# Kernel optimization log

Measured on AMD Instinct MI355X. Metric: run time of the kernel, lower is better.

## Reference

```python
import jax, jax.numpy as jnp
import numpy as np

NUM_NODES = 100000
MAX_DEGREE = 128
NODE_DIM = 256
VERT_NUM = 16384
NUM_SAMPLES = 32


def setup_inputs() -> dict:
    key = jax.random.key(0)
    k1, k2, k3, k4, k5 = jax.random.split(key, 5)
    ids = jax.random.randint(k1, (VERT_NUM,), 0, NUM_NODES, dtype=jnp.int32)
    unif_rand = jax.random.randint(k2, (NUM_SAMPLES,), 0, MAX_DEGREE, dtype=jnp.int32)
    adj_info = jax.random.randint(k3, (NUM_NODES, MAX_DEGREE), 0, NUM_NODES, dtype=jnp.int32)
    features = jax.random.normal(k4, (NUM_NODES, NODE_DIM), dtype=jnp.float32)
    W = jax.random.normal(k5, (NODE_DIM, NODE_DIM), dtype=jnp.float32) / np.sqrt(NODE_DIM)
    b = jnp.zeros((NODE_DIM,), dtype=jnp.float32)
    return {"ids": ids, "unif_rand": unif_rand, "adj_info": adj_info,
            "features": features, "W": W, "b": b}


def reference(ids, unif_rand, adj_info, features, W, b):
    num_nodes = adj_info.shape[0]
    sentinel = num_nodes - 1  # padding / "no neighbor" id

    # gather neighbor lists for the batch, then subsample columns uniformly
    adj_lists = adj_info[ids]                 # [V, max_degree]
    adj_lists = adj_lists[:, unif_rand]       # [V, S]

    # gather features
    v_f = features[ids]                       # [V, D]
    n_f = features[adj_lists]                 # [V, S, D]

    # linear sampler branch: dense projection then batched dot with neighbors
    l = v_f @ W + b                           # [V, D]
    out = jax.nn.relu(jnp.einsum('vd,vsd->vs', l, n_f))  # [V, S]

    out_mean = jnp.mean(out, axis=1)          # [V]

    # drop neighbors that are the sentinel or whose score exceeds 0.5*mean
    condition = (adj_lists == sentinel) | (out > 0.5 * out_mean[:, None])
    adj_out = jnp.where(condition, jnp.int32(sentinel), adj_lists)     # [V, S]
    adj_lists_numnz = jnp.sum(jnp.where(condition, 0.0, 1.0), axis=1)  # [V]
    att_lists = jnp.ones(adj_out.shape, dtype=jnp.float32)

    return adj_out, att_lists, adj_lists_numnz, out_mean
```

## Files before the change

kernel.cpp:

```cpp
#include <hip/hip_runtime.h>

#define NUM_NODES 100000
#define MAX_DEGREE 128
#define NODE_DIM 256
#define VERT_NUM 16384
#define NUM_SAMPLES 32
#define SENTINEL (NUM_NODES - 1)

#define VPB 8
#define NBLK (VERT_NUM / VPB)

#define ADJ_OFF 0
#define ATT_OFF (VERT_NUM * NUM_SAMPLES)
#define NNZ_OFF (2 * VERT_NUM * NUM_SAMPLES)
#define MEAN_OFF (2 * VERT_NUM * NUM_SAMPLES + VERT_NUM)

__device__ __forceinline__ float bfbits2f(unsigned int bits16) {
    return __uint_as_float(bits16 << 16);
}

__device__ __forceinline__ int probe_isf32(const void* p) {
    const unsigned int* fu = (const unsigned int*)p;
    int cnt = 0;
    for (int i = 0; i < 64; ++i) {
        const unsigned int w = fu[i];
        const unsigned int e2 = (w >> 7) & 0xFFu;
        if (e2 >= 90u && e2 <= 140u && (w & 0xFFFFu) != 0u) ++cnt;
    }
    return (cnt >= 40) ? 0 : 1;
}

template <int ISF32>
__device__ __forceinline__ float ld1(const void* p, size_t idx) {
    if (ISF32) return ((const float*)p)[idx];
    return bfbits2f(((const unsigned short*)p)[idx]);
}

template <int ISF32>
__device__ __forceinline__ float4 load4(const void* p, size_t idx) {
    if (ISF32) {
        return *(const float4*)((const float*)p + idx);
    } else {
        const ushort4 u = *(const ushort4*)((const unsigned short*)p + idx);
        float4 v;
        v.x = bfbits2f(u.x); v.y = bfbits2f(u.y);
        v.z = bfbits2f(u.z); v.w = bfbits2f(u.w);
        return v;
    }
}

template <int ISF32>
__device__ __forceinline__ void body(
    const int* __restrict__ adj_info,
    const void* __restrict__ features,
    const void* __restrict__ W,
    const void* __restrict__ bias,
    float* __restrict__ out,
    float (*AL_s)[NODE_DIM + 4],
    const int* s_ids,
    const int* s_ur,
    int (*s_adj)[NUM_SAMPLES],
    float (*s_out)[NUM_SAMPLES],
    int tid, int v0)
{
    #pragma unroll
    for (int i = 0; i < 2; ++i) {
        const int idx = tid + i * 256;
        const int r = idx >> 6;
        const int cg = (idx & 63) * 4;
        const float4 v = load4<ISF32>(features, (size_t)s_ids[r] * NODE_DIM + cg);
        *(float4*)&AL_s[r][cg] = v;
    }
    {
        const int r = tid >> 5;
        const int s = tid & 31;
        s_adj[r][s] = adj_info[(size_t)s_ids[r] * MAX_DEGREE + s_ur[s]];
    }
    __syncthreads();

    double acc[VPB];
    {
        const int col = tid;
        #pragma unroll
        for (int g = 0; g < VPB; ++g) acc[g] = 0.0;
        float wn0 = ld1<ISF32>(W, (size_t)0 * NODE_DIM + col);
        float wn1 = ld1<ISF32>(W, (size_t)1 * NODE_DIM + col);
        float wn2 = ld1<ISF32>(W, (size_t)2 * NODE_DIM + col);
        float wn3 = ld1<ISF32>(W, (size_t)3 * NODE_DIM + col);
        #pragma unroll 2
        for (int k = 0; k < NODE_DIM; k += 4) {
            const double w0 = (double)wn0;
            const double w1 = (double)wn1;
            const double w2 = (double)wn2;
            const double w3 = (double)wn3;
            if (k + 4 < NODE_DIM) {
                wn0 = ld1<ISF32>(W, (size_t)(k + 4) * NODE_DIM + col);
                wn1 = ld1<ISF32>(W, (size_t)(k + 5) * NODE_DIM + col);
                wn2 = ld1<ISF32>(W, (size_t)(k + 6) * NODE_DIM + col);
                wn3 = ld1<ISF32>(W, (size_t)(k + 7) * NODE_DIM + col);
            }
            #pragma unroll
            for (int g = 0; g < VPB; ++g) {
                const float4 a = *(const float4*)&AL_s[g][k];
                acc[g] = fma((double)a.x, w0, acc[g]);
                acc[g] = fma((double)a.y, w1, acc[g]);
                acc[g] = fma((double)a.z, w2, acc[g]);
                acc[g] = fma((double)a.w, w3, acc[g]);
            }
        }
    }
    __syncthreads();
    {
        const int col = tid;
        const double bv = (double)ld1<ISF32>(bias, col);
        #pragma unroll
        for (int g = 0; g < VPB; ++g) AL_s[g][col] = (float)(acc[g] + bv);
    }
    __syncthreads();

    {
        const int q = tid >> 4;
        const int ln = tid & 15;
        const int g = q >> 1;
        const int so = (q & 1) * 16;
        const int ln4 = ln * 4;
        const float4 Lv0 = *(const float4*)&AL_s[g][  0 + ln4];
        const float4 Lv1 = *(const float4*)&AL_s[g][ 64 + ln4];
        const float4 Lv2 = *(const float4*)&AL_s[g][128 + ln4];
        const float4 Lv3 = *(const float4*)&AL_s[g][192 + ln4];
        const int* adjq = s_adj[g];

        float4 fA0, fA1, fA2, fA3, fB0, fB1, fB2, fB3;

#define EIN_LOAD(B0, B1, B2, B3, SIDX) do {                                 \
            const size_t b_ = (size_t)adjq[(SIDX)] * NODE_DIM + ln4;        \
            B0 = load4<ISF32>(features, b_ +   0);                          \
            B1 = load4<ISF32>(features, b_ +  64);                          \
            B2 = load4<ISF32>(features, b_ + 128);                          \
            B3 = load4<ISF32>(features, b_ + 192);                          \
        } while (0)

#define EIN_COMPUTE(B0, B1, B2, B3, SIDX) do {                              \
            double a_ = 0.0;                                                \
            a_ = fma((double)B0.x, (double)Lv0.x, a_);                      \
            a_ = fma((double)B0.y, (double)Lv0.y, a_);                      \
            a_ = fma((double)B0.z, (double)Lv0.z, a_);                      \
            a_ = fma((double)B0.w, (double)Lv0.w, a_);                      \
            a_ = fma((double)B1.x, (double)Lv1.x, a_);                      \
            a_ = fma((double)B1.y, (double)Lv1.y, a_);                      \
            a_ = fma((double)B1.z, (double)Lv1.z, a_);                      \
            a_ = fma((double)B1.w, (double)Lv1.w, a_);                      \
            a_ = fma((double)B2.x, (double)Lv2.x, a_);                      \
            a_ = fma((double)B2.y, (double)Lv2.y, a_);                      \
            a_ = fma((double)B2.z, (double)Lv2.z, a_);                      \
            a_ = fma((double)B2.w, (double)Lv2.w, a_);                      \
            a_ = fma((double)B3.x, (double)Lv3.x, a_);                      \
            a_ = fma((double)B3.y, (double)Lv3.y, a_);                      \
            a_ = fma((double)B3.z, (double)Lv3.z, a_);                      \
            a_ = fma((double)B3.w, (double)Lv3.w, a_);                      \
            a_ += __shfl_xor(a_, 8);                                        \
            a_ += __shfl_xor(a_, 4);                                        \
            a_ += __shfl_xor(a_, 2);                                        \
            a_ += __shfl_xor(a_, 1);                                        \
            if (ln == 0) s_out[g][(SIDX)] = (float)a_;                      \
        } while (0)

        EIN_LOAD(fA0, fA1, fA2, fA3, so + 0);
        #pragma unroll
        for (int si = 0; si < 16; si += 2) {
            EIN_LOAD(fB0, fB1, fB2, fB3, so + si + 1);
            EIN_COMPUTE(fA0, fA1, fA2, fA3, so + si);
            if (si + 2 < 16) EIN_LOAD(fA0, fA1, fA2, fA3, so + si + 2);
            EIN_COMPUTE(fB0, fB1, fB2, fB3, so + si + 1);
        }
#undef EIN_LOAD
#undef EIN_COMPUTE
    }
    __syncthreads();

    if (tid < VPB * 16) {
        const int q = tid >> 4;
        const int ln = tid & 15;
        const int v = v0 + q;
        const float o0 = fmaxf(s_out[q][ln], 0.0f);
        const float o1 = fmaxf(s_out[q][ln + 16], 0.0f);
        double ss = (double)o0 + (double)o1;
        ss += __shfl_xor(ss, 8);
        ss += __shfl_xor(ss, 4);
        ss += __shfl_xor(ss, 2);
        ss += __shfl_xor(ss, 1);
        const float mean = (float)(ss * (1.0 / 32.0));
        const float thr = 0.5f * mean;
        const int n0 = s_adj[q][ln];
        const int n1 = s_adj[q][ln + 16];
        const bool c0 = (n0 == SENTINEL) || (o0 > thr);
        const bool c1 = (n1 == SENTINEL) || (o1 > thr);
        const size_t ob = (size_t)v * NUM_SAMPLES;
        out[ADJ_OFF + ob + ln]      = c0 ? (float)SENTINEL : (float)n0;
        out[ADJ_OFF + ob + ln + 16] = c1 ? (float)SENTINEL : (float)n1;
        out[ATT_OFF + ob + ln]      = 1.0f;
        out[ATT_OFF + ob + ln + 16] = 1.0f;
        int nz = (c0 ? 0 : 1) + (c1 ? 0 : 1);
        nz += __shfl_xor(nz, 8);
        nz += __shfl_xor(nz, 4);
        nz += __shfl_xor(nz, 2);
        nz += __shfl_xor(nz, 1);
        if (ln == 0) {
            out[NNZ_OFF + v] = (float)nz;
            out[MEAN_OFF + v] = mean;
        }
    }
}

__global__ __launch_bounds__(256, 6)
void FastMLNeighborSampler___9337258901923_kernel(
    const int* ids,
    const int* unif_rand,
    const int* adj_info,
    const void* features_raw,
    const void* W_raw,
    const void* bias_raw,
    float* out) {
    __shared__ float AL_s[VPB][NODE_DIM + 4];
    __shared__ int s_ids[VPB];
    __shared__ int s_ur[NUM_SAMPLES];
    __shared__ int s_adj[VPB][NUM_SAMPLES];
    __shared__ float s_out[VPB][NUM_SAMPLES];
    __shared__ int s_isf32;

    const int tid = threadIdx.x;
    const int v0 = blockIdx.x * VPB;

    if (tid == 0) s_isf32 = probe_isf32(features_raw);
    if (tid < VPB) {
        s_ids[tid] = ids[v0 + tid];
    } else if (tid < VPB + NUM_SAMPLES) {
        s_ur[tid - VPB] = unif_rand[tid - VPB];
    }
    __syncthreads();

    if (s_isf32) {
        body<1>(adj_info, features_raw, W_raw, bias_raw, out,
                AL_s, s_ids, s_ur, s_adj, s_out, tid, v0);
    } else {
        body<0>(adj_info, features_raw, W_raw, bias_raw, out,
                AL_s, s_ids, s_ur, s_adj, s_out, tid, v0);
    }
}

extern "C" void kernel_launch(void* const* d_in, const int* in_sizes, int n_in,
                              void* d_out, int out_size, void* d_ws, size_t ws_size,
                              hipStream_t stream) {
    const int* ids = nullptr;
    const int* unif_rand = nullptr;
    const int* adj_info = nullptr;
    const void* features = nullptr;
    const void* W = nullptr;
    const void* bias = nullptr;
    for (int i = 0; i < n_in; ++i) {
        switch (in_sizes[i]) {
            case VERT_NUM:               ids       = (const int*)d_in[i]; break;
            case NUM_SAMPLES:            unif_rand = (const int*)d_in[i]; break;
            case NUM_NODES * MAX_DEGREE: adj_info  = (const int*)d_in[i]; break;
            case NUM_NODES * NODE_DIM:   features  = (const void*)d_in[i]; break;
            case NODE_DIM * NODE_DIM:    W         = (const void*)d_in[i]; break;
            case NODE_DIM:               bias      = (const void*)d_in[i]; break;
            default: break;
        }
    }
    if (!ids || !unif_rand || !adj_info || !features || !W || !bias) {
        ids       = (const int*)d_in[0];
        unif_rand = (const int*)d_in[1];
        adj_info  = (const int*)d_in[2];
        features  = (const void*)d_in[3];
        W         = (const void*)d_in[4];
        bias      = (const void*)d_in[5];
    }
    float* out = (float*)d_out;

    FastMLNeighborSampler___9337258901923_kernel<<<NBLK, 256, 0, stream>>>(
        ids, unif_rand, adj_info, features, W, bias, out);
}
```

Baseline: 270.8 us.

## Retile projection as 2 columns x 4 vertices per thread with double-precision LDS

Changes the projection GEMM mapping so each thread computes two output columns for four vertices instead of one column for eight vertices. This halves the per-block W loads, which are now float2 loads. Vertex features are pre-converted to double in shared memory through a union with the float output buffer, which removes the repeated float-to-double conversions in the inner loop. The cost is a larger shared-memory footprint (about 16KB), which may reduce occupancy.

```diff
diff --git a/kernel.cpp b/kernel.cpp
--- a/kernel.cpp
+++ b/kernel.cpp
@@ -34,6 +34,16 @@
 __device__ __forceinline__ float ld1(const void* p, size_t idx) {
     if (ISF32) return ((const float*)p)[idx];
     return bfbits2f(((const unsigned short*)p)[idx]);
+}
+
+template <int ISF32>
+__device__ __forceinline__ float2 load2(const void* p, size_t idx) {
+    if (ISF32) {
+        return *(const float2*)((const float*)p + idx);
+    } else {
+        const ushort2 u = *(const ushort2*)((const unsigned short*)p + idx);
+        return make_float2(bfbits2f(u.x), bfbits2f(u.y));
+    }
 }
 
 template <int ISF32>
@@ -49,6 +59,11 @@
     }
 }
 
+union ALUnion {
+    double ad[VPB][NODE_DIM + 2];
+    float  lf[VPB][NODE_DIM + 4];
+};
+
 template <int ISF32>
 __device__ __forceinline__ void body(
     const int* __restrict__ adj_info,
@@ -56,7 +71,7 @@
     const void* __restrict__ W,
     const void* __restrict__ bias,
     float* __restrict__ out,
-    float (*AL_s)[NODE_DIM + 4],
+    ALUnion* __restrict__ u,
     const int* s_ids,
     const int* s_ur,
     int (*s_adj)[NUM_SAMPLES],
@@ -64,12 +79,13 @@
     int tid, int v0)
 {
     #pragma unroll
-    for (int i = 0; i < 2; ++i) {
+    for (int i = 0; i < 4; ++i) {
         const int idx = tid + i * 256;
-        const int r = idx >> 6;
-        const int cg = (idx & 63) * 4;
-        const float4 v = load4<ISF32>(features, (size_t)s_ids[r] * NODE_DIM + cg);
-        *(float4*)&AL_s[r][cg] = v;
+        const int r = idx >> 7;
+        const int dc = (idx & 127) * 2;
+        const float2 v = load2<ISF32>(features, (size_t)s_ids[r] * NODE_DIM + dc);
+        u->ad[r][dc]     = (double)v.x;
+        u->ad[r][dc + 1] = (double)v.y;
     }
     {
         const int r = tid >> 5;
@@ -78,43 +94,54 @@
     }
     __syncthreads();
 
-    double acc[VPB];
     {
-        const int col = tid;
+        const int h  = tid >> 7;
+        const int c2 = (tid & 127) * 2;
+        const int g0 = h * 4;
+        double acc[4][2];
         #pragma unroll
-        for (int g = 0; g < VPB; ++g) acc[g] = 0.0;
-        float wn0 = ld1<ISF32>(W, (size_t)0 * NODE_DIM + col);
-        float wn1 = ld1<ISF32>(W, (size_t)1 * NODE_DIM + col);
-        float wn2 = ld1<ISF32>(W, (size_t)2 * NODE_DIM + col);
-        float wn3 = ld1<ISF32>(W, (size_t)3 * NODE_DIM + col);
+        for (int g = 0; g < 4; ++g) { acc[g][0] = 0.0; acc[g][1] = 0.0; }
+
+        float2 wn0 = load2<ISF32>(W, (size_t)0 * NODE_DIM + c2);
+        float2 wn1 = load2<ISF32>(W, (size_t)1 * NODE_DIM + c2);
+        float2 wn2 = load2<ISF32>(W, (size_t)2 * NODE_DIM + c2);
+        float2 wn3 = load2<ISF32>(W, (size_t)3 * NODE_DIM + c2);
         #pragma unroll 2
         for (int k = 0; k < NODE_DIM; k += 4) {
-            const double w0 = (double)wn0;
-            const double w1 = (double)wn1;
-            const double w2 = (double)wn2;
-            const double w3 = (double)wn3;
+            const double w00 = (double)wn0.x, w01 = (double)wn0.y;
+            const double w10 = (double)wn1.x, w11 = (double)wn1.y;
+            const double w20 = (double)wn2.x, w21 = (double)wn2.y;
+            const double w30 = (double)wn3.x, w31 = (double)wn3.y;
             if (k + 4 < NODE_DIM) {
-                wn0 = ld1<ISF32>(W, (size_t)(k + 4) * NODE_DIM + col);
-                wn1 = ld1<ISF32>(W, (size_t)(k + 5) * NODE_DIM + col);
-                wn2 = ld1<ISF32>(W, (size_t)(k + 6) * NODE_DIM + col);
-                wn3 = ld1<ISF32>(W, (size_t)(k + 7) * NODE_DIM + col);
+                wn0 = load2<ISF32>(W, (size_t)(k + 4) * NODE_DIM + c2);
+                wn1 = load2<ISF32>(W, (size_t)(k + 5) * NODE_DIM + c2);
+                wn2 = load2<ISF32>(W, (size_t)(k + 6) * NODE_DIM + c2);
+                wn3 = load2<ISF32>(W, (size_t)(k + 7) * NODE_DIM + c2);
             }
             #pragma unroll
-            for (int g = 0; g < VPB; ++g) {
-                const float4 a = *(const float4*)&AL_s[g][k];
-                acc[g] = fma((double)a.x, w0, acc[g]);
-                acc[g] = fma((double)a.y, w1, acc[g]);
-                acc[g] = fma((double)a.z, w2, acc[g]);
-                acc[g] = fma((double)a.w, w3, acc[g]);
+            for (int g = 0; g < 4; ++g) {
+                const double2 a01 = *(const double2*)&u->ad[g0 + g][k];
+                const double2 a23 = *(const double2*)&u->ad[g0 + g][k + 2];
+                acc[g][0] = fma(a01.x, w00, acc[g][0]);
+                acc[g][0] = fma(a01.y, w10, acc[g][0]);
+                acc[g][0] = fma(a23.x, w20, acc[g][0]);
+                acc[g][0] = fma(a23.y, w30, acc[g][0]);
+                acc[g][1] = fma(a01.x, w01, acc[g][1]);
+                acc[g][1] = fma(a01.y, w11, acc[g][1]);
+                acc[g][1] = fma(a23.x, w21, acc[g][1]);
+                acc[g][1] = fma(a23.y, w31, acc[g][1]);
             }
         }
-    }
-    __syncthreads();
-    {
-        const int col = tid;
-        const double bv = (double)ld1<ISF32>(bias, col);
-        #pragma unroll
-        for (int g = 0; g < VPB; ++g) AL_s[g][col] = (float)(acc[g] + bv);
+        __syncthreads();
+        {
+            const double b0 = (double)ld1<ISF32>(bias, c2);
+            const double b1 = (double)ld1<ISF32>(bias, (size_t)c2 + 1);
+            #pragma unroll
+            for (int g = 0; g < 4; ++g) {
+                u->lf[g0 + g][c2]     = (float)(acc[g][0] + b0);
+                u->lf[g0 + g][c2 + 1] = (float)(acc[g][1] + b1);
+            }
+        }
     }
     __syncthreads();
 
@@ -124,10 +151,10 @@
         const int g = q >> 1;
         const int so = (q & 1) * 16;
         const int ln4 = ln * 4;
-        const float4 Lv0 = *(const float4*)&AL_s[g][  0 + ln4];
-        const float4 Lv1 = *(const float4*)&AL_s[g][ 64 + ln4];
-        const float4 Lv2 = *(const float4*)&AL_s[g][128 + ln4];
-        const float4 Lv3 = *(const float4*)&AL_s[g][192 + ln4];
+        const float4 Lv0 = *(const float4*)&u->lf[g][  0 + ln4];
+        const float4 Lv1 = *(const float4*)&u->lf[g][ 64 + ln4];
+        const float4 Lv2 = *(const float4*)&u->lf[g][128 + ln4];
+        const float4 Lv3 = *(const float4*)&u->lf[g][192 + ln4];
         const int* adjq = s_adj[g];
 
         float4 fA0, fA1, fA2, fA3, fB0, fB1, fB2, fB3;
@@ -221,7 +248,7 @@
     const void* W_raw,
     const void* bias_raw,
     float* out) {
-    __shared__ float AL_s[VPB][NODE_DIM + 4];
+    __shared__ ALUnion uAL;
     __shared__ int s_ids[VPB];
     __shared__ int s_ur[NUM_SAMPLES];
     __shared__ int s_adj[VPB][NUM_SAMPLES];
@@ -241,10 +268,10 @@
 
     if (s_isf32) {
         body<1>(adj_info, features_raw, W_raw, bias_raw, out,
-                AL_s, s_ids, s_ur, s_adj, s_out, tid, v0);
+                &uAL, s_ids, s_ur, s_adj, s_out, tid, v0);
     } else {
         body<0>(adj_info, features_raw, W_raw, bias_raw, out,
-                AL_s, s_ids, s_ur, s_adj, s_out, tid, v0);
+                &uAL, s_ids, s_ur, s_adj, s_out, tid, v0);
     }
 }
 
```

Result: slower. 315.2 us (+16.4%).

## Warp-specialize block into matmul and gather-einsum pipeline stages with double buffering

Applied to the files above, without the earlier changes.

Each block now handles 16 vertices in two tiles of 8 and runs 512 threads. Warps 0-3 compute the dense projection for tile t while warps 4-7 do the neighbor-gather dot products and the thresholding for tile t-1, with double-buffered shared memory for the inputs and projections. The epilogue is folded into the einsum warps using a ballot/popcount instead of a separate pass. This aims to overlap the FP64 matmul with the memory-bound feature gathers. The cost is that each group idles during the pipeline fill and drain, the block uses more shared memory, and there are half as many blocks.

```diff
diff --git a/kernel.cpp b/kernel.cpp
--- a/kernel.cpp
+++ b/kernel.cpp
@@ -7,8 +7,11 @@
 #define NUM_SAMPLES 32
 #define SENTINEL (NUM_NODES - 1)
 
-#define VPB 8
-#define NBLK (VERT_NUM / VPB)
+#define TVPB 8
+#define TILES 2
+#define VPBLK (TVPB * TILES)
+#define NBLK (VERT_NUM / VPBLK)
+#define NTHR 512
 
 #define ADJ_OFF 0
 #define ATT_OFF (VERT_NUM * NUM_SAMPLES)
@@ -51,168 +54,191 @@
 
 template <int ISF32>
 __device__ __forceinline__ void body(
+    const int* __restrict__ ids,
     const int* __restrict__ adj_info,
     const void* __restrict__ features,
     const void* __restrict__ W,
     const void* __restrict__ bias,
     float* __restrict__ out,
-    float (*AL_s)[NODE_DIM + 4],
-    const int* s_ids,
+    float (*bufA)[TVPB][NODE_DIM + 4],
+    float (*bufL)[TVPB][NODE_DIM + 4],
+    int (*s_adj)[TVPB][NUM_SAMPLES],
     const int* s_ur,
-    int (*s_adj)[NUM_SAMPLES],
-    float (*s_out)[NUM_SAMPLES],
-    int tid, int v0)
+    int tid, int v_blk)
 {
-    #pragma unroll
-    for (int i = 0; i < 2; ++i) {
-        const int idx = tid + i * 256;
-        const int r = idx >> 6;
-        const int cg = (idx & 63) * 4;
-        const float4 v = load4<ISF32>(features, (size_t)s_ids[r] * NODE_DIM + cg);
-        *(float4*)&AL_s[r][cg] = v;
-    }
     {
-        const int r = tid >> 5;
-        const int s = tid & 31;
-        s_adj[r][s] = adj_info[(size_t)s_ids[r] * MAX_DEGREE + s_ur[s]];
-    }
+        const int r = tid >> 6;
+        const int cg = (tid & 63) * 4;
+        const float4 v = load4<ISF32>(features, (size_t)ids[v_blk + r] * NODE_DIM + cg);
+        *(float4*)&bufA[0][r][cg] = v;
+        if (tid < 256) {
+            const int rr = tid >> 5;
+            const int ss = tid & 31;
+            s_adj[0][rr][ss] = adj_info[(size_t)ids[v_blk + rr] * MAX_DEGREE + s_ur[ss]];
+        }
+    }
+    const int ur_mm = s_ur[tid & 31];
     __syncthreads();
 
-    double acc[VPB];
-    {
-        const int col = tid;
-        #pragma unroll
-        for (int g = 0; g < VPB; ++g) acc[g] = 0.0;
-        float wn0 = ld1<ISF32>(W, (size_t)0 * NODE_DIM + col);
-        float wn1 = ld1<ISF32>(W, (size_t)1 * NODE_DIM + col);
-        float wn2 = ld1<ISF32>(W, (size_t)2 * NODE_DIM + col);
-        float wn3 = ld1<ISF32>(W, (size_t)3 * NODE_DIM + col);
-        #pragma unroll 2
-        for (int k = 0; k < NODE_DIM; k += 4) {
-            const double w0 = (double)wn0;
-            const double w1 = (double)wn1;
-            const double w2 = (double)wn2;
-            const double w3 = (double)wn3;
-            if (k + 4 < NODE_DIM) {
-                wn0 = ld1<ISF32>(W, (size_t)(k + 4) * NODE_DIM + col);
-                wn1 = ld1<ISF32>(W, (size_t)(k + 5) * NODE_DIM + col);
-                wn2 = ld1<ISF32>(W, (size_t)(k + 6) * NODE_DIM + col);
-                wn3 = ld1<ISF32>(W, (size_t)(k + 7) * NODE_DIM + col);
+    int cur = 0;
+    for (int s = 0; s < TILES + 1; ++s) {
+        if (tid < 256) {
+            const int mmtile = s;
+            if (mmtile < TILES) {
+                const bool do_stage = (mmtile + 1 < TILES);
+                float4 st0, st1;
+                int adjv = 0;
+                if (do_stage) {
+                    const int v0n = v_blk + (mmtile + 1) * TVPB;
+                    const int i0 = tid;
+                    const int i1 = tid + 256;
+                    st0 = load4<ISF32>(features,
+                        (size_t)ids[v0n + (i0 >> 6)] * NODE_DIM + (i0 & 63) * 4);
+                    st1 = load4<ISF32>(features,
+                        (size_t)ids[v0n + (i1 >> 6)] * NODE_DIM + (i1 & 63) * 4);
+                    adjv = adj_info[(size_t)ids[v0n + (tid >> 5)] * MAX_DEGREE + ur_mm];
+                }
+
+                {
+                    const int col = tid;
+                    double acc[TVPB];
+                    #pragma unroll
+                    for (int g = 0; g < TVPB; ++g) acc[g] = 0.0;
+                    float wn0 = ld1<ISF32>(W, (size_t)0 * NODE_DIM + col);
+                    float wn1 = ld1<ISF32>(W, (size_t)1 * NODE_DIM + col);
+                    float wn2 = ld1<ISF32>(W, (size_t)2 * NODE_DIM + col);
+                    float wn3 = ld1<ISF32>(W, (size_t)3 * NODE_DIM + col);
+                    #pragma unroll 2
+                    for (int k = 0; k < NODE_DIM; k += 4) {
+                        const double w0 = (double)wn0;
+                        const double w1 = (double)wn1;
+                        const double w2 = (double)wn2;
+                        const double w3 = (double)wn3;
+                        if (k + 4 < NODE_DIM) {
+                            wn0 = ld1<ISF32>(W, (size_t)(k + 4) * NODE_DIM + col);
+                            wn1 = ld1<ISF32>(W, (size_t)(k + 5) * NODE_DIM + col);
+                            wn2 = ld1<ISF32>(W, (size_t)(k + 6) * NODE_DIM + col);
+                            wn3 = ld1<ISF32>(W, (size_t)(k + 7) * NODE_DIM + col);
+                        }
+                        #pragma unroll
+                        for (int g = 0; g < TVPB; ++g) {
+                            const float4 a = *(const float4*)&bufA[cur][g][k];
+                            acc[g] = fma((double)a.x, w0, acc[g]);
+                            acc[g] = fma((double)a.y, w1, acc[g]);
+                            acc[g] = fma((double)a.z, w2, acc[g]);
+                            acc[g] = fma((double)a.w, w3, acc[g]);
+                        }
+                    }
+                    const double bv = (double)ld1<ISF32>(bias, (size_t)col);
+                    #pragma unroll
+                    for (int g = 0; g < TVPB; ++g)
+                        bufL[cur][g][col] = (float)(acc[g] + bv);
+                }
+
+                if (do_stage) {
+                    const int nxt = cur ^ 1;
+                    const int i0 = tid, i1 = tid + 256;
+                    *(float4*)&bufA[nxt][i0 >> 6][(i0 & 63) * 4] = st0;
+                    *(float4*)&bufA[nxt][i1 >> 6][(i1 & 63) * 4] = st1;
+                    s_adj[nxt][tid >> 5][tid & 31] = adjv;
+                }
             }
-            #pragma unroll
-            for (int g = 0; g < VPB; ++g) {
-                const float4 a = *(const float4*)&AL_s[g][k];
-                acc[g] = fma((double)a.x, w0, acc[g]);
-                acc[g] = fma((double)a.y, w1, acc[g]);
-                acc[g] = fma((double)a.z, w2, acc[g]);
-                acc[g] = fma((double)a.w, w3, acc[g]);
+        } else {
+            const int eintile = s - 1;
+            if (eintile >= 0) {
+                const int prev = cur ^ 1;
+                const int we = (tid >> 6) - 4;
+                const int lane = tid & 63;
+                const int q2 = lane >> 4;
+                const int ln = lane & 15;
+                const int g = we * 2 + (q2 >> 1);
+                const int so = (q2 & 1) * 16;
+                const int ln4 = ln * 4;
+                const float4 Lv0 = *(const float4*)&bufL[prev][g][  0 + ln4];
+                const float4 Lv1 = *(const float4*)&bufL[prev][g][ 64 + ln4];
+                const float4 Lv2 = *(const float4*)&bufL[prev][g][128 + ln4];
+                const float4 Lv3 = *(const float4*)&bufL[prev][g][192 + ln4];
+                const int* adjq = s_adj[prev][g];
+                float kf = 0.0f;
+
+                float4 fA0, fA1, fA2, fA3, fB0, fB1, fB2, fB3;
+
+#define EIN_LOAD(B0, B1, B2, B3, SIDX) do {                                 \
+                const size_t b_ = (size_t)adjq[(SIDX)] * NODE_DIM + ln4;    \
+                B0 = load4<ISF32>(features, b_ +   0);                      \
+                B1 = load4<ISF32>(features, b_ +  64);                      \
+                B2 = load4<ISF32>(features, b_ + 128);                      \
+                B3 = load4<ISF32>(features, b_ + 192);                      \
+            } while (0)
+
+#define EIN_COMPUTE(B0, B1, B2, B3, SILOC) do {                             \
+                double a_ = 0.0;                                            \
+                a_ = fma((double)B0.x, (double)Lv0.x, a_);                  \
+                a_ = fma((double)B0.y, (double)Lv0.y, a_);                  \
+                a_ = fma((double)B0.z, (double)Lv0.z, a_);                  \
+                a_ = fma((double)B0.w, (double)Lv0.w, a_);                  \
+                a_ = fma((double)B1.x, (double)Lv1.x, a_);                  \
+                a_ = fma((double)B1.y, (double)Lv1.y, a_);                  \
+                a_ = fma((double)B1.z, (double)Lv1.z, a_);                  \
+                a_ = fma((double)B1.w, (double)Lv1.w, a_);                  \
+                a_ = fma((double)B2.x, (double)Lv2.x, a_);                  \
+                a_ = fma((double)B2.y, (double)Lv2.y, a_);                  \
+                a_ = fma((double)B2.z, (double)Lv2.z, a_);                  \
+                a_ = fma((double)B2.w, (double)Lv2.w, a_);                  \
+                a_ = fma((double)B3.x, (double)Lv3.x, a_);                  \
+                a_ = fma((double)B3.y, (double)Lv3.y, a_);                  \
+                a_ = fma((double)B3.z, (double)Lv3.z, a_);                  \
+                a_ = fma((double)B3.w, (double)Lv3.w, a_);                  \
+                a_ += __shfl_xor(a_, 8);                                    \
+                a_ += __shfl_xor(a_, 4);                                    \
+                a_ += __shfl_xor(a_, 2);                                    \
+                a_ += __shfl_xor(a_, 1);                                    \
+                kf = ((SILOC) == ln) ? (float)a_ : kf;                      \
+            } while (0)
+
+                EIN_LOAD(fA0, fA1, fA2, fA3, so + 0);
+                #pragma unroll
+                for (int si = 0; si < 16; si += 2) {
+                    EIN_LOAD(fB0, fB1, fB2, fB3, so + si + 1);
+                    EIN_COMPUTE(fA0, fA1, fA2, fA3, si);
+                    if (si + 2 < 16) EIN_LOAD(fA0, fA1, fA2, fA3, so + si + 2);
+                    EIN_COMPUTE(fB0, fB1, fB2, fB3, si + 1);
+                }
+#undef EIN_LOAD
+#undef EIN_COMPUTE
+
+                const float o = fmaxf(kf, 0.0f);
+                const double od = (double)o;
+                const double oo = __shfl_xor(od, 16);
+                double ssum = od + oo;
+                ssum += __shfl_xor(ssum, 8);
+                ssum += __shfl_xor(ssum, 4);
+                ssum += __shfl_xor(ssum, 2);
+                ssum += __shfl_xor(ssum, 1);
+                const float mean = (float)(ssum * (1.0 / 32.0));
+                const float thr = 0.5f * mean;
+                const int sl = lane & 31;
+                const int nb = adjq[sl];
+                const bool c = (nb == SENTINEL) || (o > thr);
+                const int v = v_blk + eintile * TVPB + g;
+                const size_t ob = (size_t)v * NUM_SAMPLES;
+                out[ADJ_OFF + ob + sl] = c ? (float)SENTINEL : (float)nb;
+                out[ATT_OFF + ob + sl] = 1.0f;
+                const unsigned long long bal = __ballot(!c);
+                if (sl == 0) {
+                    const unsigned long long m =
+                        (lane < 32) ? 0xFFFFFFFFull : 0xFFFFFFFF00000000ull;
+                    out[NNZ_OFF + v] = (float)__popcll(bal & m);
+                    out[MEAN_OFF + v] = mean;
+                }
             }
         }
-    }
-    __syncthreads();
-    {
-        const int col = tid;
-        const double bv = (double)ld1<ISF32>(bias, col);
-        #pragma unroll
-        for (int g = 0; g < VPB; ++g) AL_s[g][col] = (float)(acc[g] + bv);
-    }
-    __syncthreads();
-
-    {
-        const int q = tid >> 4;
-        const int ln = tid & 15;
-        const int g = q >> 1;
-        const int so = (q & 1) * 16;
-        const int ln4 = ln * 4;
-        const float4 Lv0 = *(const float4*)&AL_s[g][  0 + ln4];
-        const float4 Lv1 = *(const float4*)&AL_s[g][ 64 + ln4];
-        const float4 Lv2 = *(const float4*)&AL_s[g][128 + ln4];
-        const float4 Lv3 = *(const float4*)&AL_s[g][192 + ln4];
-        const int* adjq = s_adj[g];
-
-        float4 fA0, fA1, fA2, fA3, fB0, fB1, fB2, fB3;
-
-#define EIN_LOAD(B0, B1, B2, B3, SIDX) do {                                 \
-            const size_t b_ = (size_t)adjq[(SIDX)] * NODE_DIM + ln4;        \
-            B0 = load4<ISF32>(features, b_ +   0);                          \
-            B1 = load4<ISF32>(features, b_ +  64);                          \
-            B2 = load4<ISF32>(features, b_ + 128);                          \
-            B3 = load4<ISF32>(features, b_ + 192);                          \
-        } while (0)
-
-#define EIN_COMPUTE(B0, B1, B2, B3, SIDX) do {                              \
-            double a_ = 0.0;                                                \
-            a_ = fma((double)B0.x, (double)Lv0.x, a_);                      \
-            a_ = fma((double)B0.y, (double)Lv0.y, a_);                      \
-            a_ = fma((double)B0.z, (double)Lv0.z, a_);                      \
-            a_ = fma((double)B0.w, (double)Lv0.w, a_);                      \
-            a_ = fma((double)B1.x, (double)Lv1.x, a_);                      \
-            a_ = fma((double)B1.y, (double)Lv1.y, a_);                      \
-            a_ = fma((double)B1.z, (double)Lv1.z, a_);                      \
-            a_ = fma((double)B1.w, (double)Lv1.w, a_);                      \
-            a_ = fma((double)B2.x, (double)Lv2.x, a_);                      \
-            a_ = fma((double)B2.y, (double)Lv2.y, a_);                      \
-            a_ = fma((double)B2.z, (double)Lv2.z, a_);                      \
-            a_ = fma((double)B2.w, (double)Lv2.w, a_);                      \
-            a_ = fma((double)B3.x, (double)Lv3.x, a_);                      \
-            a_ = fma((double)B3.y, (double)Lv3.y, a_);                      \
-            a_ = fma((double)B3.z, (double)Lv3.z, a_);                      \
-            a_ = fma((double)B3.w, (double)Lv3.w, a_);                      \
-            a_ += __shfl_xor(a_, 8);                                        \
-            a_ += __shfl_xor(a_, 4);                                        \
-            a_ += __shfl_xor(a_, 2);                                        \
-            a_ += __shfl_xor(a_, 1);                                        \
-            if (ln == 0) s_out[g][(SIDX)] = (float)a_;                      \
-        } while (0)
-
-        EIN_LOAD(fA0, fA1, fA2, fA3, so + 0);
-        #pragma unroll
-        for (int si = 0; si < 16; si += 2) {
-            EIN_LOAD(fB0, fB1, fB2, fB3, so + si + 1);
-            EIN_COMPUTE(fA0, fA1, fA2, fA3, so + si);
-            if (si + 2 < 16) EIN_LOAD(fA0, fA1, fA2, fA3, so + si + 2);
-            EIN_COMPUTE(fB0, fB1, fB2, fB3, so + si + 1);
-        }
-#undef EIN_LOAD
-#undef EIN_COMPUTE
-    }
-    __syncthreads();
-
-    if (tid < VPB * 16) {
-        const int q = tid >> 4;
-        const int ln = tid & 15;
-        const int v = v0 + q;
-        const float o0 = fmaxf(s_out[q][ln], 0.0f);
-        const float o1 = fmaxf(s_out[q][ln + 16], 0.0f);
-        double ss = (double)o0 + (double)o1;
-        ss += __shfl_xor(ss, 8);
-        ss += __shfl_xor(ss, 4);
-        ss += __shfl_xor(ss, 2);
-        ss += __shfl_xor(ss, 1);
-        const float mean = (float)(ss * (1.0 / 32.0));
-        const float thr = 0.5f * mean;
-        const int n0 = s_adj[q][ln];
-        const int n1 = s_adj[q][ln + 16];
-        const bool c0 = (n0 == SENTINEL) || (o0 > thr);
-        const bool c1 = (n1 == SENTINEL) || (o1 > thr);
-        const size_t ob = (size_t)v * NUM_SAMPLES;
-        out[ADJ_OFF + ob + ln]      = c0 ? (float)SENTINEL : (float)n0;
-        out[ADJ_OFF + ob + ln + 16] = c1 ? (float)SENTINEL : (float)n1;
-        out[ATT_OFF + ob + ln]      = 1.0f;
-        out[ATT_OFF + ob + ln + 16] = 1.0f;
-        int nz = (c0 ? 0 : 1) + (c1 ? 0 : 1);
-        nz += __shfl_xor(nz, 8);
-        nz += __shfl_xor(nz, 4);
-        nz += __shfl_xor(nz, 2);
-        nz += __shfl_xor(nz, 1);
-        if (ln == 0) {
-            out[NNZ_OFF + v] = (float)nz;
-            out[MEAN_OFF + v] = mean;
-        }
-    }
-}
-
-__global__ __launch_bounds__(256, 6)
+        __syncthreads();
+        cur ^= 1;
+    }
+}
+
+__global__ __launch_bounds__(NTHR, 6)
 void FastMLNeighborSampler___9337258901923_kernel(
     const int* ids,
     const int* unif_rand,
@@ -221,30 +247,25 @@
     const void* W_raw,
     const void* bias_raw,
     float* out) {
-    __shared__ float AL_s[VPB][NODE_DIM + 4];
-    __shared__ int s_ids[VPB];
+    __shared__ float bufA[2][TVPB][NODE_DIM + 4];
+    __shared__ float bufL[2][TVPB][NODE_DIM + 4];
+    __shared__ int s_adj[2][TVPB][NUM_SAMPLES];
     __shared__ int s_ur[NUM_SAMPLES];
-    __shared__ int s_adj[VPB][NUM_SAMPLES];
-    __shared__ float s_out[VPB][NUM_SAMPLES];
     __shared__ int s_isf32;
 
     const int tid = threadIdx.x;
-    const int v0 = blockIdx.x * VPB;
+    const int v_blk = blockIdx.x * VPBLK;
 
     if (tid == 0) s_isf32 = probe_isf32(features_raw);
-    if (tid < VPB) {
-        s_ids[tid] = ids[v0 + tid];
-    } else if (tid < VPB + NUM_SAMPLES) {
-        s_ur[tid - VPB] = unif_rand[tid - VPB];
-    }
+    if (tid < NUM_SAMPLES) s_ur[tid] = unif_rand[tid];
     __syncthreads();
 
     if (s_isf32) {
-        body<1>(adj_info, features_raw, W_raw, bias_raw, out,
-                AL_s, s_ids, s_ur, s_adj, s_out, tid, v0);
+        body<1>(ids, adj_info, features_raw, W_raw, bias_raw, out,
+                bufA, bufL, s_adj, s_ur, tid, v_blk);
     } else {
-        body<0>(adj_info, features_raw, W_raw, bias_raw, out,
-                AL_s, s_ids, s_ur, s_adj, s_out, tid, v0);
+        body<0>(ids, adj_info, features_raw, W_raw, bias_raw, out,
+                bufA, bufL, s_adj, s_ur, tid, v_blk);
     }
 }
 
@@ -278,6 +299,6 @@
     }
     float* out = (float*)d_out;
 
-    FastMLNeighborSampler___9337258901923_kernel<<<NBLK, 256, 0, stream>>>(
+    FastMLNeighborSampler___9337258901923_kernel<<<NBLK, NTHR, 0, stream>>>(
         ids, unif_rand, adj_info, features, W, bias, out);
 }
```

New measurement: 341.9 us. 26.2% more time.

## Remap neighbor dot products to one wavefront per vertex pair with deeper prefetch

Applied to the files above, without the earlier changes.

The einsum stage now gives each wavefront two vertices and has each lane load one float4 of a full 256-wide feature row. This replaces the old scheme of 16-lane groups loading four float4s per row. A rolling window of eight in-flight row loads overlaps gather latency with the reduction, which now takes six shuffle steps instead of four. Launch bounds drop from 6 to 4 waves per SIMD so the extra prefetch registers fit, which may reduce occupancy.

```diff
diff --git a/kernel.cpp b/kernel.cpp
--- a/kernel.cpp
+++ b/kernel.cpp
@@ -112,69 +112,84 @@
     __syncthreads();
     {
         const int col = tid;
-        const double bv = (double)ld1<ISF32>(bias, col);
+        const double bv = (double)ld1<ISF32>(bias, (size_t)col);
         #pragma unroll
         for (int g = 0; g < VPB; ++g) AL_s[g][col] = (float)(acc[g] + bv);
     }
     __syncthreads();
 
     {
-        const int q = tid >> 4;
-        const int ln = tid & 15;
-        const int g = q >> 1;
-        const int so = (q & 1) * 16;
-        const int ln4 = ln * 4;
-        const float4 Lv0 = *(const float4*)&AL_s[g][  0 + ln4];
-        const float4 Lv1 = *(const float4*)&AL_s[g][ 64 + ln4];
-        const float4 Lv2 = *(const float4*)&AL_s[g][128 + ln4];
-        const float4 Lv3 = *(const float4*)&AL_s[g][192 + ln4];
-        const int* adjq = s_adj[g];
-
-        float4 fA0, fA1, fA2, fA3, fB0, fB1, fB2, fB3;
-
-#define EIN_LOAD(B0, B1, B2, B3, SIDX) do {                                 \
-            const size_t b_ = (size_t)adjq[(SIDX)] * NODE_DIM + ln4;        \
-            B0 = load4<ISF32>(features, b_ +   0);                          \
-            B1 = load4<ISF32>(features, b_ +  64);                          \
-            B2 = load4<ISF32>(features, b_ + 128);                          \
-            B3 = load4<ISF32>(features, b_ + 192);                          \
-        } while (0)
-
-#define EIN_COMPUTE(B0, B1, B2, B3, SIDX) do {                              \
-            double a_ = 0.0;                                                \
-            a_ = fma((double)B0.x, (double)Lv0.x, a_);                      \
-            a_ = fma((double)B0.y, (double)Lv0.y, a_);                      \
-            a_ = fma((double)B0.z, (double)Lv0.z, a_);                      \
-            a_ = fma((double)B0.w, (double)Lv0.w, a_);                      \
-            a_ = fma((double)B1.x, (double)Lv1.x, a_);                      \
-            a_ = fma((double)B1.y, (double)Lv1.y, a_);                      \
-            a_ = fma((double)B1.z, (double)Lv1.z, a_);                      \
-            a_ = fma((double)B1.w, (double)Lv1.w, a_);                      \
-            a_ = fma((double)B2.x, (double)Lv2.x, a_);                      \
-            a_ = fma((double)B2.y, (double)Lv2.y, a_);                      \
-            a_ = fma((double)B2.z, (double)Lv2.z, a_);                      \
-            a_ = fma((double)B2.w, (double)Lv2.w, a_);                      \
-            a_ = fma((double)B3.x, (double)Lv3.x, a_);                      \
-            a_ = fma((double)B3.y, (double)Lv3.y, a_);                      \
-            a_ = fma((double)B3.z, (double)Lv3.z, a_);                      \
-            a_ = fma((double)B3.w, (double)Lv3.w, a_);                      \
-            a_ += __shfl_xor(a_, 8);                                        \
-            a_ += __shfl_xor(a_, 4);                                        \
-            a_ += __shfl_xor(a_, 2);                                        \
-            a_ += __shfl_xor(a_, 1);                                        \
-            if (ln == 0) s_out[g][(SIDX)] = (float)a_;                      \
-        } while (0)
-
-        EIN_LOAD(fA0, fA1, fA2, fA3, so + 0);
-        #pragma unroll
-        for (int si = 0; si < 16; si += 2) {
-            EIN_LOAD(fB0, fB1, fB2, fB3, so + si + 1);
-            EIN_COMPUTE(fA0, fA1, fA2, fA3, so + si);
-            if (si + 2 < 16) EIN_LOAD(fA0, fA1, fA2, fA3, so + si + 2);
-            EIN_COMPUTE(fB0, fB1, fB2, fB3, so + si + 1);
-        }
-#undef EIN_LOAD
-#undef EIN_COMPUTE
+        const int wv = tid >> 6;
+        const int lane = tid & 63;
+        const int g0v = wv * 2;
+        const int g1v = g0v + 1;
+        const int l4 = lane * 4;
+        const int* adj0 = s_adj[g0v];
+        const int* adj1 = s_adj[g1v];
+        float4 Lv = *(const float4*)&AL_s[g0v][l4];
+        float4 f0, f1, f2, f3, f4, f5, f6, f7;
+
+#define LOADR(B, ADJ, S) do {                                               \
+        B = load4<ISF32>(features, (size_t)(ADJ)[(S)] * NODE_DIM + l4);     \
+    } while (0)
+
+#define COMPS(B, G, S) do {                                                 \
+        double a_ = 0.0;                                                    \
+        a_ = fma((double)B.x, (double)Lv.x, a_);                            \
+        a_ = fma((double)B.y, (double)Lv.y, a_);                            \
+        a_ = fma((double)B.z, (double)Lv.z, a_);                            \
+        a_ = fma((double)B.w, (double)Lv.w, a_);                            \
+        a_ += __shfl_xor(a_, 1);                                            \
+        a_ += __shfl_xor(a_, 2);                                            \
+        a_ += __shfl_xor(a_, 4);                                            \
+        a_ += __shfl_xor(a_, 8);                                            \
+        a_ += __shfl_xor(a_, 16);                                           \
+        a_ += __shfl_xor(a_, 32);                                           \
+        if (lane == 0) s_out[(G)][(S)] = (float)a_;                         \
+    } while (0)
+
+#define PAIR(B, G, S, ADJ, NS) do { COMPS(B, G, S); LOADR(B, ADJ, NS); } while (0)
+
+#define BLOCK8(G, S0, ADJ, N0)                                              \
+        PAIR(f0, G, (S0) + 0, ADJ, (N0) + 0);                               \
+        PAIR(f1, G, (S0) + 1, ADJ, (N0) + 1);                               \
+        PAIR(f2, G, (S0) + 2, ADJ, (N0) + 2);                               \
+        PAIR(f3, G, (S0) + 3, ADJ, (N0) + 3);                               \
+        PAIR(f4, G, (S0) + 4, ADJ, (N0) + 4);                               \
+        PAIR(f5, G, (S0) + 5, ADJ, (N0) + 5);                               \
+        PAIR(f6, G, (S0) + 6, ADJ, (N0) + 6);                               \
+        PAIR(f7, G, (S0) + 7, ADJ, (N0) + 7);
+
+#define BLOCK8_END(G, S0)                                                   \
+        COMPS(f0, G, (S0) + 0);                                             \
+        COMPS(f1, G, (S0) + 1);                                             \
+        COMPS(f2, G, (S0) + 2);                                             \
+        COMPS(f3, G, (S0) + 3);                                             \
+        COMPS(f4, G, (S0) + 4);                                             \
+        COMPS(f5, G, (S0) + 5);                                             \
+        COMPS(f6, G, (S0) + 6);                                             \
+        COMPS(f7, G, (S0) + 7);
+
+        LOADR(f0, adj0, 0); LOADR(f1, adj0, 1);
+        LOADR(f2, adj0, 2); LOADR(f3, adj0, 3);
+        LOADR(f4, adj0, 4); LOADR(f5, adj0, 5);
+        LOADR(f6, adj0, 6); LOADR(f7, adj0, 7);
+
+        BLOCK8(g0v,  0, adj0,  8)
+        BLOCK8(g0v,  8, adj0, 16)
+        BLOCK8(g0v, 16, adj0, 24)
+        BLOCK8(g0v, 24, adj1,  0)
+        Lv = *(const float4*)&AL_s[g1v][l4];
+        BLOCK8(g1v,  0, adj1,  8)
+        BLOCK8(g1v,  8, adj1, 16)
+        BLOCK8(g1v, 16, adj1, 24)
+        BLOCK8_END(g1v, 24)
+
+#undef LOADR
+#undef COMPS
+#undef PAIR
+#undef BLOCK8
+#undef BLOCK8_END
     }
     __syncthreads();
 
@@ -212,7 +227,7 @@
     }
 }
 
-__global__ __launch_bounds__(256, 6)
+__global__ __launch_bounds__(256, 4)
 void FastMLNeighborSampler___9337258901923_kernel(
     const int* ids,
     const int* unif_rand,
```

Result: slower. 289.3 us (+6.8%).
